# Performance work log

Hardware: AMD Instinct MI355X
Metric: run time of the kernel (lower is better)

## Reference

```python
import jax, jax.numpy as jnp
import numpy as np

N_HEAD = 16
N_KV_HEAD = 4
HEAD_DIM = 128
D_MODEL = 2048
ROTARY_DIM = 128  # == head_dim
ROTARY_BASE = 10000
N_CTX = 2048
BATCH = 2
SEQ = 2048


def _rope_sincos(T, dtype):
    # Matches calculate_sin_cos_rotary with rotary_adjacent_pairs=False:
    # freq = base**(d/(rd/2)) for d in [0, rd/2), then tiled twice.
    pos = jnp.arange(T, dtype=jnp.float32)
    dim = jnp.arange(ROTARY_DIM // 2, dtype=jnp.float32)
    freq = jnp.asarray(ROTARY_BASE, jnp.float32) ** (dim / (ROTARY_DIM / 2))
    freq = jnp.concatenate([freq, freq])          # [rd]
    angles = pos[:, None] / freq[None, :]          # [T, rd]
    return jnp.sin(angles).astype(dtype), jnp.cos(angles).astype(dtype)


def _rotate_half(x):
    # rotate_every_two with adjacent_pairs=False: [-x2, x1] over halves
    n = x.shape[-1] // 2
    return jnp.concatenate([-x[..., n:], x[..., :n]], axis=-1)


def setup_inputs() -> dict:
    key = jax.random.key(0)
    kx, kq, kkv, kp = jax.random.split(key, 4)
    scale = 0.02
    return {
        "x": jax.random.normal(kx, (BATCH, SEQ, D_MODEL), jnp.float32),
        "Wq": jax.random.normal(kq, (D_MODEL, D_MODEL), jnp.float32) * scale,
        "Wkv": jax.random.normal(kkv, (2 * N_KV_HEAD * HEAD_DIM, D_MODEL), jnp.float32) * scale,
        "Wproj": jax.random.normal(kp, (D_MODEL, D_MODEL), jnp.float32) * scale,
    }


def reference(x, Wq, Wkv, Wproj):
    B, T, C = x.shape
    # QKV projections (torch Linear: y = x @ W.T)
    q = x @ Wq.T                                   # [B,T,C]
    kv = x @ Wkv.T                                 # [B,T,2*kv*hd]
    k, v = jnp.split(kv, 2, axis=2)
    q = q.reshape(B, T, N_HEAD, HEAD_DIM).transpose(0, 2, 1, 3)      # [B,H,T,d]
    k = k.reshape(B, T, N_KV_HEAD, HEAD_DIM).transpose(0, 2, 1, 3)   # [B,Hk,T,d]
    v = v.reshape(B, T, N_KV_HEAD, HEAD_DIM).transpose(0, 2, 1, 3)

    # RoPE: position_ids = arange(T) clamped at n_ctx-1 (identity for T<=n_ctx)
    sin, cos = _rope_sincos(T, q.dtype)            # [T, rd]
    sin = sin[None, None]                          # [1,1,T,rd]
    cos = cos[None, None]
    q = q * cos + _rotate_half(q) * sin
    k = k * cos + _rotate_half(k) * sin

    # GQA: expand kv heads (repeat_interleave along head dim)
    rep = N_HEAD // N_KV_HEAD
    k = jnp.repeat(k, rep, axis=1)                 # [B,H,T,d]
    v = jnp.repeat(v, rep, axis=1)

    # Causal SDPA
    scale = 1.0 / np.sqrt(HEAD_DIM)
    scores = jnp.einsum('bhqd,bhkd->bhqk', q, k) * scale
    causal = jnp.tril(jnp.ones((T, T), bool))
    scores = jnp.where(causal[None, None], scores, jnp.asarray(-jnp.inf, scores.dtype))
    attn = jax.nn.softmax(scores, axis=-1)
    y = jnp.einsum('bhqk,bhkd->bhqd', attn, v)     # [B,H,T,d]

    y = y.transpose(0, 2, 1, 3).reshape(B, T, C)
    return y @ Wproj.T
```

## Files before the change

### kernel.cpp

```cpp
#include <hip/hip_runtime.h>
#include <stdint.h>

#define T_SEQ 2048
#define D_MODEL 2048
#define N_KV 4
#define HD 128
#define QKV_W 3072

typedef unsigned short us;
typedef __attribute__((ext_vector_type(8))) short bf16x8;
typedef __attribute__((ext_vector_type(4))) float f32x4;
typedef __attribute__((ext_vector_type(8))) unsigned short u16x8;

__device__ __forceinline__ us f2bf(float f) {
  union { float f; unsigned int u; } v; v.f = f;
  unsigned int r = v.u + 0x7FFFu + ((v.u >> 16) & 1u);
  return (us)(r >> 16);
}
__device__ __forceinline__ float bf2f(us h) {
  union { unsigned int u; float f; } v; v.u = ((unsigned int)h) << 16;
  return v.f;
}

__device__ __forceinline__ void load_lds16(const void* g, void* l) {
  __builtin_amdgcn_global_load_lds(
      (const __attribute__((address_space(1))) void*)g,
      (__attribute__((address_space(3))) void*)l, 16, 0, 0);
}

__global__ void fill_diag(float* __restrict__ out, float val, int n) {
  int i = blockIdx.x * blockDim.x + threadIdx.x;
  if (i < n) out[i] = val;
}

__global__ void cast_f32_bf16(const float* __restrict__ src,
                              us* __restrict__ dst, int n8) {
  int i = blockIdx.x * blockDim.x + threadIdx.x;
  if (i >= n8) return;
  const float4* s = (const float4*)src + (size_t)i * 2;
  float4 a = s[0], b = s[1];
  u16x8 o;
  o[0] = f2bf(a.x); o[1] = f2bf(a.y); o[2] = f2bf(a.z); o[3] = f2bf(a.w);
  o[4] = f2bf(b.x); o[5] = f2bf(b.y); o[6] = f2bf(b.z); o[7] = f2bf(b.w);
  *((u16x8*)dst + i) = o;
}

template <typename OUT>
__global__ __launch_bounds__(256) void gemm_bt(
    const us* __restrict__ A, const us* __restrict__ B,
    OUT* __restrict__ C, int M, int N, int K) {
  __shared__ us As[2][128 * 32];
  __shared__ us Bs[2][128 * 32];

  const int tid  = threadIdx.x;
  const int lane = tid & 63;
  const int wave = tid >> 6;
  const int l15  = lane & 15;
  const int quad = lane >> 4;
  const int bm = blockIdx.x * 128;
  const int bn = blockIdx.y * 128;
  const int wm = (wave & 1) * 64;
  const int wn = (wave >> 1) * 64;

  f32x4 acc[4][4];
#pragma unroll
  for (int i = 0; i < 4; i++)
#pragma unroll
    for (int j = 0; j < 4; j++) acc[i][j] = (f32x4)0.f;

  const int srow = tid >> 2;
  const int scol = (tid & 3) * 8;
  const us* Ag = A + (size_t)(bm + srow) * K + scol;
  const us* Bg = B + (size_t)(bn + srow) * K + scol;
  const size_t rowskip = (size_t)64 * K;

#define STAGE(buf, koff)                                            \
  do {                                                              \
    load_lds16(Ag + (koff), &As[(buf)][tid * 8]);                   \
    load_lds16(Ag + (koff) + rowskip, &As[(buf)][tid * 8 + 2048]);  \
    load_lds16(Bg + (koff), &Bs[(buf)][tid * 8]);                   \
    load_lds16(Bg + (koff) + rowskip, &Bs[(buf)][tid * 8 + 2048]);  \
  } while (0)

  STAGE(0, 0);
  __syncthreads();

  int cur = 0;
  for (int k0 = 0; k0 < K; k0 += 32) {
    if (k0 + 32 < K) STAGE(cur ^ 1, k0 + 32);

    bf16x8 a[4], b[4];
#pragma unroll
    for (int mt = 0; mt < 4; mt++)
      a[mt] = *(const bf16x8*)&As[cur][(wm + mt * 16 + l15) * 32 + quad * 8];
#pragma unroll
    for (int nt = 0; nt < 4; nt++)
      b[nt] = *(const bf16x8*)&Bs[cur][(wn + nt * 16 + l15) * 32 + quad * 8];
#pragma unroll
    for (int mt = 0; mt < 4; mt++)
#pragma unroll
      for (int nt = 0; nt < 4; nt++)
        acc[mt][nt] = __builtin_amdgcn_mfma_f32_16x16x32_bf16(a[mt], b[nt], acc[mt][nt], 0, 0, 0);

    __syncthreads();
    cur ^= 1;
  }
#undef STAGE

#pragma unroll
  for (int mt = 0; mt < 4; mt++) {
    int row = bm + wm + mt * 16 + quad * 4;
#pragma unroll
    for (int nt = 0; nt < 4; nt++) {
      int col = bn + wn + nt * 16 + l15;
#pragma unroll
      for (int r = 0; r < 4; r++) {
        if constexpr (sizeof(OUT) == 4)
          C[(size_t)(row + r) * N + col] = acc[mt][nt][r];
        else
          C[(size_t)(row + r) * N + col] = f2bf(acc[mt][nt][r]);
      }
    }
  }
}

#define GBAR()                                  \
  do {                                          \
    asm volatile("" ::: "memory");              \
    __builtin_amdgcn_s_barrier();               \
    asm volatile("" ::: "memory");              \
  } while (0)
#define VMCNT6() asm volatile("s_waitcnt vmcnt(6)" ::: "memory")
#define VMCNT0() asm volatile("s_waitcnt vmcnt(0)" ::: "memory")

template <typename OUT>
__global__ __launch_bounds__(512) void gemm_bt8(
    const us* __restrict__ A, const us* __restrict__ B,
    OUT* __restrict__ C, int M, int N, int K) {
  __shared__ us As[2][16384];
  __shared__ us Bs[2][16384];

  const int tid  = threadIdx.x;
  const int lane = tid & 63;
  const int wave = tid >> 6;
  const int wm   = wave & 1;
  const int wn   = wave >> 1;
  const int l15  = lane & 15;
  const int quad = lane >> 4;
  const int bm = blockIdx.x * 256;
  const int bn = blockIdx.y * 256;
  const int wm8 = wm * 8;
  const int wn4 = wn * 4;

  const int ro = ((l15 << 5) | (quad << 3)) ^ ((l15 & 8) << 1);

  const int s    = lane ^ ((lane & 32) >> 4);
  const int srow = s >> 2;
  const int schk = (s & 3) * 8;

  const int R_Ae = (wave & 3) | ((wave & 4) << 1);
  const int R_Al = R_Ae + 4;
  const int R_Be = ((wave >> 1) << 2) | (wave & 1);
  const int R_Bl = R_Be + 2;

  const us* Ab = A + (size_t)bm * K;
  const us* Bb = B + (size_t)bn * K;

  f32x4 acc[8][4];
#pragma unroll
  for (int i = 0; i < 8; i++)
#pragma unroll
    for (int j = 0; j < 4; j++) acc[i][j] = (f32x4)0.f;

  bf16x8 af[4][2], bf[4][2];

#define STG(DST, PG, R, KT)                                                   \
  do {                                                                        \
    load_lds16((PG) + (size_t)((R) * 16 + srow) * K + (KT) * 64 + schk,       \
               &(DST)[(((R) * 2 + 0) << 9) + (lane << 3)]);                   \
    load_lds16((PG) + (size_t)((R) * 16 + srow) * K + (KT) * 64 + 32 + schk,  \
               &(DST)[(((R) * 2 + 1) << 9) + (lane << 3)]);                   \
  } while (0)

#define LDA4(BUF, MTB)                                                        \
  _Pragma("unroll") for (int t = 0; t < 4; t++)                               \
      _Pragma("unroll") for (int ks = 0; ks < 2; ks++)                        \
          af[t][ks] = *(const bf16x8*)&As[BUF][(((wm8 + (MTB) + t) * 2 + ks)  \
                                               << 9) + ro];

#define LDB2(BUF, NTB)                                                        \
  _Pragma("unroll") for (int t = 0; t < 2; t++)                               \
      _Pragma("unroll") for (int ks = 0; ks < 2; ks++)                        \
          bf[(NTB) + t][ks] = *(const bf16x8*)&Bs[BUF][                       \
              (((wn4 + (NTB) + t) * 2 + ks) << 9) + ro];

#define MQ(MH, NB)                                                            \
  __builtin_amdgcn_s_setprio(1);                                              \
  _Pragma("unroll") for (int t = 0; t < 4; t++)                               \
      _Pragma("unroll") for (int u = 0; u < 2; u++)                           \
          _Pragma("unroll") for (int ks = 0; ks < 2; ks++)                    \
              acc[(MH) * 4 + t][(NB) + u] =                                   \
                  __builtin_amdgcn_mfma_f32_16x16x32_bf16(                    \
                      af[t][ks], bf[(NB) + u][ks],                            \
                      acc[(MH) * 4 + t][(NB) + u], 0, 0, 0);                  \
  __builtin_amdgcn_s_setprio(0);

  STG(As[0], Ab, R_Ae, 0); STG(As[0], Ab, R_Al, 0);
  STG(Bs[0], Bb, R_Be, 0); STG(Bs[0], Bb, R_Bl, 0);
  STG(As[1], Ab, R_Ae, 1); STG(Bs[1], Bb, R_Be, 1); STG(Bs[1], Bb, R_Bl, 1);
  VMCNT6();
  GBAR();

  const int NI = K >> 7;
  for (int i = 0; i < NI - 1; i++) {
    const int t0 = 2 * i;
    LDA4(0, 0) LDB2(0, 0)
    STG(As[1], Ab, R_Al, t0 + 1);
    GBAR(); MQ(0, 0) GBAR();
    LDB2(0, 2)
    STG(As[0], Ab, R_Ae, t0 + 2);
    GBAR(); MQ(0, 2) GBAR();
    LDA4(0, 4)
    STG(Bs[0], Bb, R_Be, t0 + 2);
    GBAR(); MQ(1, 2) GBAR();
    STG(Bs[0], Bb, R_Bl, t0 + 2);
    GBAR(); MQ(1, 0) VMCNT6(); GBAR();
    LDA4(1, 0) LDB2(1, 0)
    STG(As[0], Ab, R_Al, t0 + 2);
    GBAR(); MQ(0, 0) GBAR();
    LDB2(1, 2)
    STG(As[1], Ab, R_Ae, t0 + 3);
    GBAR(); MQ(0, 2) GBAR();
    LDA4(1, 4)
    STG(Bs[1], Bb, R_Be, t0 + 3);
    GBAR(); MQ(1, 2) GBAR();
    STG(Bs[1], Bb, R_Bl, t0 + 3);
    GBAR(); MQ(1, 0) VMCNT6(); GBAR();
  }
  {
    const int t0 = 2 * NI - 2;
    LDA4(0, 0) LDB2(0, 0)
    STG(As[1], Ab, R_Al, t0 + 1);
    GBAR(); MQ(0, 0) GBAR();
    LDB2(0, 2)
    GBAR(); MQ(0, 2) GBAR();
    LDA4(0, 4)
    GBAR(); MQ(1, 2) GBAR();
    GBAR(); MQ(1, 0) VMCNT0(); GBAR();
    LDA4(1, 0) LDB2(1, 0)
    GBAR(); MQ(0, 0) GBAR();
    LDB2(1, 2)
    GBAR(); MQ(0, 2) GBAR();
    LDA4(1, 4)
    GBAR(); MQ(1, 2) GBAR();
    MQ(1, 0)
  }
#undef STG
#undef LDA4
#undef LDB2
#undef MQ

#pragma unroll
  for (int mt = 0; mt < 8; mt++) {
    int row = bm + wm * 128 + mt * 16 + quad * 4;
#pragma unroll
    for (int nt = 0; nt < 4; nt++) {
      int col = bn + wn * 64 + nt * 16 + l15;
#pragma unroll
      for (int r = 0; r < 4; r++) {
        if constexpr (sizeof(OUT) == 4)
          C[(size_t)(row + r) * N + col] = acc[mt][nt][r];
        else
          C[(size_t)(row + r) * N + col] = f2bf(acc[mt][nt][r]);
      }
    }
  }
}

__global__ void rope_kernel(us* __restrict__ qkv) {
  const int row = blockIdx.x;
  const int t = row & (T_SEQ - 1);
  const int tid = threadIdx.x;
  const float L2_10K_64 = 13.287712379549449f / 64.f;
  us* rp = qkv + (size_t)row * QKV_W;

#pragma unroll
  for (int it = 0; it < 4; it++) {
    int idx = it * 256 + tid;
    int h = idx >> 6, i = idx & 63;
    int base = h * HD;
    float ang = (float)t * exp2f(-(float)i * L2_10K_64);
    float s, c; sincosf(ang, &s, &c);
    float x1 = bf2f(rp[base + i]);
    float x2 = bf2f(rp[base + i + 64]);
    rp[base + i]      = f2bf(x1 * c - x2 * s);
    rp[base + i + 64] = f2bf(x2 * c + x1 * s);
  }
  {
    int h = tid >> 6, i = tid & 63;
    int base = 2048 + h * HD;
    float ang = (float)t * exp2f(-(float)i * L2_10K_64);
    float s, c; sincosf(ang, &s, &c);
    float x1 = bf2f(rp[base + i]);
    float x2 = bf2f(rp[base + i + 64]);
    rp[base + i]      = f2bf(x1 * c - x2 * s);
    rp[base + i + 64] = f2bf(x2 * c + x1 * s);
  }
}

__device__ __forceinline__ int vperm(int d) { return ((d >> 3) ^ d) & 7; }

__global__ __launch_bounds__(512) void attn_kernel(
    const us* __restrict__ qkv, us* __restrict__ y) {
  __shared__ us Ks[64][136];
  __shared__ us Vt[128][64];
  __shared__ us Pl[8][2][16][40];

  const int tid  = threadIdx.x;
  const int lane = tid & 63;
  const int wave = tid >> 6;
  const int l15  = lane & 15;
  const int quad = lane >> 4;
  const int bh = blockIdx.y;
  const int b  = bh >> 4;
  const int h  = bh & 15;
  const int hk = h >> 2;
  const int p  = blockIdx.x ^ (b * 15);
  const int xA = 31 - p;
  const int xB = p;
  const int x_mine = (wave < 4) ? xA : xB;
  const int m0 = x_mine * 64;
  const int w4 = wave & 3;

  const us* base = qkv + (size_t)b * T_SEQ * QKV_W;
  const int kcol = 2048 + hk * HD;
  const int vcol = kcol + 512;
  const int skey = tid >> 4;
  const int skk  = (tid & 15) * 8;
  const float scale = 0.12751744f;

  bf16x8 qf[4];
  {
    const us* Qrow = base + (size_t)(m0 + w4 * 16 + l15) * QKV_W + h * HD;
#pragma unroll
    for (int s = 0; s < 4; s++)
      qf[s] = *(const bf16x8*)&Qrow[s * 32 + quad * 8];
  }

  f32x4 O[8];
#pragma unroll
  for (int i = 0; i < 8; i++) O[i] = (f32x4)0.f;
  float mrun[4], lrun[4];
#pragma unroll
  for (int r = 0; r < 4; r++) { mrun[r] = -INFINITY; lrun[r] = 0.f; }

  uint4 kreg[2]; u16x8 vreg[2];
#pragma unroll
  for (int r = 0; r < 2; r++) {
    const us* row = base + (size_t)(skey + r * 32) * QKV_W;
    kreg[r] = *(const uint4*)(row + kcol + skk);
    vreg[r] = *(const u16x8*)(row + vcol + skk);
  }

  for (int j = 0; j <= xA; j++) {
    __syncthreads();
#pragma unroll
    for (int r = 0; r < 2; r++) {
      int key = skey + r * 32;
      *(uint4*)&Ks[key][skk] = kreg[r];
#pragma unroll
      for (int i = 0; i < 8; i++) {
        int d = skk + i;
        Vt[d][key ^ (vperm(d) << 3)] = vreg[r][i];
      }
    }
    __syncthreads();

    if (j < xA) {
      const int k0n = (j + 1) * 64;
#pragma unroll
      for (int r = 0; r < 2; r++) {
        const us* row = base + (size_t)(k0n + skey + r * 32) * QKV_W;
        kreg[r] = *(const uint4*)(row + kcol + skk);
        vreg[r] = *(const u16x8*)(row + vcol + skk);
      }
    }

    if (j <= x_mine) {
      f32x4 S[4];
      __builtin_amdgcn_s_setprio(1);
#pragma unroll
      for (int nt = 0; nt < 4; nt++) {
        f32x4 sa = (f32x4)0.f;
#pragma unroll
        for (int ks = 0; ks < 4; ks++) {
          bf16x8 kf = *(const bf16x8*)&Ks[nt * 16 + l15][ks * 32 + quad * 8];
          sa = __builtin_amdgcn_mfma_f32_16x16x32_bf16(qf[ks], kf, sa, 0, 0, 0);
        }
        S[nt] = sa;
      }
      __builtin_amdgcn_s_setprio(0);

      const int row0 = m0 + w4 * 16 + quad * 4;
      if (j == x_mine) {
        const int k0 = j * 64;
#pragma unroll
        for (int nt = 0; nt < 4; nt++) {
          int col = k0 + nt * 16 + l15;
#pragma unroll
          for (int r = 0; r < 4; r++) {
            float v = S[nt][r] * scale;
            if (col > row0 + r) v = -INFINITY;
            S[nt][r] = v;
          }
        }
      } else {
#pragma unroll
        for (int nt = 0; nt < 4; nt++)
#pragma unroll
          for (int r = 0; r < 4; r++) S[nt][r] *= scale;
      }

      float pr[4][4];
#pragma unroll
      for (int r = 0; r < 4; r++) {
        float mx = fmaxf(fmaxf(S[0][r], S[1][r]), fmaxf(S[2][r], S[3][r]));
#pragma unroll
        for (int off = 1; off < 16; off <<= 1)
          mx = fmaxf(mx, __shfl_xor(mx, off, 64));
        float mnew = fmaxf(mrun[r], mx);
        float alpha = exp2f(mrun[r] - mnew);
        mrun[r] = mnew;
        float sum = 0.f;
#pragma unroll
        for (int nt = 0; nt < 4; nt++) {
          float pv = exp2f(S[nt][r] - mnew);
          pr[nt][r] = pv;
          sum += pv;
        }
        lrun[r] = lrun[r] * alpha + sum;
#pragma unroll
        for (int ot = 0; ot < 8; ot++) O[ot][r] *= alpha;
      }

#pragma unroll
      for (int kh = 0; kh < 2; kh++) {
#pragma unroll
        for (int nt = 0; nt < 2; nt++)
#pragma unroll
          for (int r = 0; r < 4; r++)
            Pl[wave][kh][quad * 4 + r][nt * 16 + l15] = f2bf(pr[kh * 2 + nt][r]);
        bf16x8 pf = *(const bf16x8*)&Pl[wave][kh][l15][quad * 8];
        __builtin_amdgcn_s_setprio(1);
#pragma unroll
        for (int ot = 0; ot < 8; ot++) {
          int dcol = ot * 16 + l15;
          bf16x8 vf = *(const bf16x8*)&Vt[dcol][(kh * 32 + quad * 8) ^ (vperm(dcol) << 3)];
          O[ot] = __builtin_amdgcn_mfma_f32_16x16x32_bf16(pf, vf, O[ot], 0, 0, 0);
        }
        __builtin_amdgcn_s_setprio(0);
      }
    }
  }

  const int t_out = m0 + w4 * 16 + quad * 4;
#pragma unroll
  for (int r = 0; r < 4; r++) {
    float s = lrun[r];
#pragma unroll
    for (int off = 1; off < 16; off <<= 1)
      s += __shfl_xor(s, off, 64);
    float inv_l = 1.f / s;
    us* yrow = y + (size_t)(b * T_SEQ + t_out + r) * D_MODEL + h * HD;
#pragma unroll
    for (int ot = 0; ot < 8; ot++)
      yrow[ot * 16 + l15] = f2bf(O[ot][r] * inv_l);
  }
}

extern "C" void kernel_launch(void* const* d_in, const int* in_sizes, int n_in,
                              void* d_out, int out_size, void* d_ws, size_t ws_size,
                              hipStream_t stream) {
  const float* x     = (const float*)d_in[0];
  const float* Wq    = (const float*)d_in[1];
  const float* Wkv   = (const float*)d_in[2];
  const float* Wproj = (const float*)d_in[3];
  float* out = (float*)d_out;

  const size_t NX  = (size_t)4096 * 2048;
  const size_t NWQ = (size_t)2048 * 2048;
  const size_t NWK = (size_t)1024 * 2048;
  const size_t needed_ws = (NX + (NWQ + NWK) + NWQ + NX) * sizeof(us);

  int b0 = (n_in >= 1 && (size_t)in_sizes[0] == NX);
  int b1 = (n_in >= 2 && (size_t)in_sizes[1] == NWQ);
  int b2 = (n_in >= 3 && (size_t)in_sizes[2] == NWK);
  int b3 = (n_in >= 4 && (size_t)in_sizes[3] == NWQ);
  int ws_ok = (ws_size >= needed_ws);
  int out_ok = ((size_t)out_size == NX);
  if (!(n_in == 4 && b0 && b1 && b2 && b3 && ws_ok && out_ok)) {
    float code = 1.0e6f * (float)(n_in < 10 ? n_in : 9)
               + 1.0e5f * b0 + 1.0e4f * b1 + 1.0e3f * b2 + 1.0e2f * b3
               + 10.0f * ws_ok + 40.0f * out_ok;
    fill_diag<<<dim3((out_size + 255) / 256), dim3(256), 0, stream>>>(out, code, out_size);
    return;
  }

  us* xb     = (us*)d_ws;
  us* Wqkvb  = xb + NX;
  us* Wpb    = Wqkvb + NWQ + NWK;
  us* ybuf   = Wpb + NWQ;
  us* qkvbuf = (us*)d_out;

  dim3 blk(256);
  cast_f32_bf16<<<dim3((int)(NX  / 8 / 256)), blk, 0, stream>>>(x,     xb,          (int)(NX  / 8));
  cast_f32_bf16<<<dim3((int)(NWQ / 8 / 256)), blk, 0, stream>>>(Wq,    Wqkvb,       (int)(NWQ / 8));
  cast_f32_bf16<<<dim3((int)(NWK / 8 / 256)), blk, 0, stream>>>(Wkv,   Wqkvb + NWQ, (int)(NWK / 8));
  cast_f32_bf16<<<dim3((int)(NWQ / 8 / 256)), blk, 0, stream>>>(Wproj, Wpb,         (int)(NWQ / 8));

  gemm_bt8<us><<<dim3(16, 12), dim3(512), 0, stream>>>(xb, Wqkvb, qkvbuf, 4096, 3072, 2048);
  rope_kernel<<<dim3(4096), blk, 0, stream>>>(qkvbuf);
  attn_kernel<<<dim3(16, 32), dim3(512), 0, stream>>>(qkvbuf, ybuf);
  gemm_bt<float><<<dim3(32, 16), blk, 0, stream>>>(ybuf, Wpb, out, 4096, 2048, 2048);
}
```

Baseline: 392.6 us.

## Pack four causal query tiles per attention block with 1024 threads

The attention kernel now uses 16 waves per block, split into four groups, and each group handles a different 64-row query tile (31-p, p, 15-p, 16+p). The four tiles share the same staged K/V tiles in LDS. This halves the grid and the number of K/V tile loads from global memory per head. Each thread now stages one K/V row instead of two. The batch-dependent XOR swizzle on blockIdx is dropped. In exchange the block size doubles, which lowers the number of resident blocks and can raise register pressure under the 1024-thread launch bound. Because the block loops to the largest tile, groups with short causal ranges sit idle at barriers.

```diff
diff --git a/kernel.cpp b/kernel.cpp
--- a/kernel.cpp
+++ b/kernel.cpp
@@ -310,11 +310,11 @@
 
 __device__ __forceinline__ int vperm(int d) { return ((d >> 3) ^ d) & 7; }
 
-__global__ __launch_bounds__(512) void attn_kernel(
+__global__ __launch_bounds__(1024) void attn_kernel(
     const us* __restrict__ qkv, us* __restrict__ y) {
   __shared__ us Ks[64][136];
   __shared__ us Vt[128][64];
-  __shared__ us Pl[8][2][16][40];
+  __shared__ us Pl[16][2][16][40];
 
   const int tid  = threadIdx.x;
   const int lane = tid & 63;
@@ -325,12 +325,15 @@
   const int b  = bh >> 4;
   const int h  = bh & 15;
   const int hk = h >> 2;
-  const int p  = blockIdx.x ^ (b * 15);
+  const int p  = blockIdx.x;
+  const int g  = wave >> 2;
+  const int w4 = wave & 3;
   const int xA = 31 - p;
-  const int xB = p;
-  const int x_mine = (wave < 4) ? xA : xB;
+  const int x_mine = (g == 0) ? (31 - p)
+                   : (g == 1) ? p
+                   : (g == 2) ? (15 - p)
+                              : (16 + p);
   const int m0 = x_mine * 64;
-  const int w4 = wave & 3;
 
   const us* base = qkv + (size_t)b * T_SEQ * QKV_W;
   const int kcol = 2048 + hk * HD;
@@ -354,36 +357,27 @@
 #pragma unroll
   for (int r = 0; r < 4; r++) { mrun[r] = -INFINITY; lrun[r] = 0.f; }
 
-  uint4 kreg[2]; u16x8 vreg[2];
-#pragma unroll
-  for (int r = 0; r < 2; r++) {
-    const us* row = base + (size_t)(skey + r * 32) * QKV_W;
-    kreg[r] = *(const uint4*)(row + kcol + skk);
-    vreg[r] = *(const u16x8*)(row + vcol + skk);
+  uint4 kreg; u16x8 vreg;
+  {
+    const us* row = base + (size_t)skey * QKV_W;
+    kreg = *(const uint4*)(row + kcol + skk);
+    vreg = *(const u16x8*)(row + vcol + skk);
   }
 
   for (int j = 0; j <= xA; j++) {
     __syncthreads();
-#pragma unroll
-    for (int r = 0; r < 2; r++) {
-      int key = skey + r * 32;
-      *(uint4*)&Ks[key][skk] = kreg[r];
-#pragma unroll
-      for (int i = 0; i < 8; i++) {
-        int d = skk + i;
-        Vt[d][key ^ (vperm(d) << 3)] = vreg[r][i];
-      }
+    *(uint4*)&Ks[skey][skk] = kreg;
+#pragma unroll
+    for (int i = 0; i < 8; i++) {
+      int d = skk + i;
+      Vt[d][skey ^ (vperm(d) << 3)] = vreg[i];
     }
     __syncthreads();
 
     if (j < xA) {
-      const int k0n = (j + 1) * 64;
-#pragma unroll
-      for (int r = 0; r < 2; r++) {
-        const us* row = base + (size_t)(k0n + skey + r * 32) * QKV_W;
-        kreg[r] = *(const uint4*)(row + kcol + skk);
-        vreg[r] = *(const u16x8*)(row + vcol + skk);
-      }
+      const us* row = base + (size_t)((j + 1) * 64 + skey) * QKV_W;
+      kreg = *(const uint4*)(row + kcol + skk);
+      vreg = *(const u16x8*)(row + vcol + skk);
     }
 
     if (j <= x_mine) {
@@ -520,6 +514,6 @@
 
   gemm_bt8<us><<<dim3(16, 12), dim3(512), 0, stream>>>(xb, Wqkvb, qkvbuf, 4096, 3072, 2048);
   rope_kernel<<<dim3(4096), blk, 0, stream>>>(qkvbuf);
-  attn_kernel<<<dim3(16, 32), dim3(512), 0, stream>>>(qkvbuf, ybuf);
+  attn_kernel<<<dim3(8, 32), dim3(1024), 0, stream>>>(qkvbuf, ybuf);
   gemm_bt<float><<<dim3(32, 16), blk, 0, stream>>>(ybuf, Wpb, out, 4096, 2048, 2048);
 }
```

Result: faster. 338.7 us (-13.7%).
